# Optimization experiments

Measured on AMD Instinct MI355X. Metric: run time of the kernel, lower is better.

Reference implementation:

```python
import jax, jax.numpy as jnp
import numpy as np

B, N, F, FE, H, C = 2, 2048, 128, 8, 4, 64
LEAKY_ALPHA = 0.2
NEG_INF = -1e9


def setup_inputs() -> dict:
    key = jax.random.key(0)
    ks = jax.random.split(key, 8)
    return {
        "X": jax.random.normal(ks[0], (B, N, F), jnp.float32),
        "A": jax.random.uniform(ks[1], (B, N, N), jnp.float32),
        "E": jax.random.normal(ks[2], (B, N, N, FE), jnp.float32),
        "W_edge": jax.random.normal(ks[3], (FE, 1), jnp.float32) * 0.1,
        "b_edge": jnp.zeros((1,), jnp.float32),
        "W_gat": jax.random.normal(ks[4], (H, F, C), jnp.float32) * 0.05,
        "a_src": jax.random.normal(ks[5], (H, C), jnp.float32) * 0.1,
        "a_dst": jax.random.normal(ks[6], (H, C), jnp.float32) * 0.1,
        "b_gat": jnp.zeros((H * C,), jnp.float32),
        "ln_gamma": jnp.ones((H * C,), jnp.float32),
        "ln_beta": jnp.zeros((H * C,), jnp.float32),
    }


def reference(X, A, E, W_edge, b_edge, W_gat, a_src, a_dst, b_gat, ln_gamma, ln_beta):
    # --- edge gate: sigmoid(Dense_1(E)) -> [B,N,N], multiply into adjacency ---
    edge_w = jax.nn.sigmoid(jnp.einsum("bije,eo->bijo", E, W_edge) + b_edge)
    A = A * edge_w[..., 0]  # [B,N,N]

    # --- multi-head dense GAT (spektral GATConv, concat_heads, elu) ---
    h = jnp.einsum("bnf,hfc->bnhc", X, W_gat)  # [B,N,H,C]
    s_src = jnp.einsum("bnhc,hc->bnh", h, a_src)  # [B,N,H]
    s_dst = jnp.einsum("bnhc,hc->bnh", h, a_dst)
    # e_ij = LeakyReLU(src_i + dst_j): [B,N(i),N(j),H]
    logits = jax.nn.leaky_relu(s_src[:, :, None, :] + s_dst[:, None, :, :],
                               negative_slope=LEAKY_ALPHA)
    mask = jnp.where(A == 0.0, NEG_INF, 0.0)[..., None]  # [B,N,N,1]
    attn = jax.nn.softmax(logits + mask, axis=2)  # softmax over neighbors j
    out = jnp.einsum("bijh,bjhc->bihc", attn, h)  # [B,N,H,C]
    out = out.reshape(B, N, H * C) + b_gat
    out = jax.nn.elu(out)

    # --- LayerNorm over the feature axis (inference: dropout is identity) ---
    mu = jnp.mean(out, axis=-1, keepdims=True)
    var = jnp.var(out, axis=-1, keepdims=True)
    out = (out - mu) * jax.lax.rsqrt(var + 1e-3) * ln_gamma + ln_beta
    return out
```

## Files before the change

### kernel.cpp

```cpp
#include <hip/hip_runtime.h>
#include <hip/hip_bf16.h>


#define BB 2
#define NN 2048
#define FF 128
#define HH 4
#define CC 64
#define HC 256
#define TN 8
#define JB (NN / 8)
#define LOG2E 1.4426950408889634f

typedef __attribute__((ext_vector_type(8))) short short8;
typedef __attribute__((ext_vector_type(4))) float f32x4;

__device__ __forceinline__ float wave_sum(float v) {
#pragma unroll
    for (int m = 32; m >= 1; m >>= 1) v += __shfl_xor(v, m, 64);
    return v;
}

__device__ __forceinline__ unsigned short bf16rne(float x) {
    unsigned u = __float_as_uint(x);
    return (unsigned short)((u + 0x7fffu + ((u >> 16) & 1u)) >> 16);
}

__global__ __launch_bounds__(256) void k1_proj(
    const float* __restrict__ X, const float* __restrict__ Adj,
    const float* __restrict__ Wg,
    const float* __restrict__ a_src, const float* __restrict__ a_dst,
    unsigned short* __restrict__ hT, float* __restrict__ ssT,
    float* __restrict__ sdT, unsigned char* __restrict__ zT)
{
    const int blk = blockIdx.x;
    const int b  = blk / (NN / TN);
    const int n0 = (blk % (NN / TN)) * TN;
    const int tid = threadIdx.x;
    const int h = tid >> 6, c = tid & 63;

    float hv[TN];
#pragma unroll
    for (int r = 0; r < TN; ++r) hv[r] = 0.f;

    const float* xp = X + (size_t)(b * NN + n0) * FF;

#pragma unroll 4
    for (int f4 = 0; f4 < FF / 4; ++f4) {
        const int f = f4 * 4;
        const float w0 = Wg[(h * FF + f + 0) * CC + c];
        const float w1 = Wg[(h * FF + f + 1) * CC + c];
        const float w2 = Wg[(h * FF + f + 2) * CC + c];
        const float w3 = Wg[(h * FF + f + 3) * CC + c];
#pragma unroll
        for (int r = 0; r < TN; ++r) {
            float4 x4 = *(const float4*)(xp + r * FF + f);
            hv[r] = fmaf(x4.x, w0, hv[r]);
            hv[r] = fmaf(x4.y, w1, hv[r]);
            hv[r] = fmaf(x4.z, w2, hv[r]);
            hv[r] = fmaf(x4.w, w3, hv[r]);
        }
    }

    union { short8 v; unsigned short u[8]; } pk;
#pragma unroll
    for (int r = 0; r < TN; ++r) pk.u[r] = bf16rne(hv[r]);
    *(short8*)&hT[((((size_t)b * HH + h) * JB + (n0 >> 3)) * CC + c) * 8] = pk.v;

    const float as = a_src[tid];
    const float ad = a_dst[tid];
#pragma unroll
    for (int r = 0; r < TN; ++r) {
        const int n = n0 + r;
        float s1 = wave_sum(hv[r] * as);
        float s2 = wave_sum(hv[r] * ad);
        if (c == 0) {
            ssT[(b * HH + h) * NN + n] = s1 * LOG2E;
            sdT[(b * HH + h) * NN + n] = s2 * LOG2E;
        }
    }

    {
        const int r = tid >> 5;
        const int s = tid & 31;
        const size_t row = (size_t)(b * NN + n0 + r);
        const float* ap = Adj + row * NN + s * 64;
        unsigned char* zp = zT + (row << 8);
#pragma unroll
        for (int k = 0; k < 8; ++k) {
            float4 a0 = *(const float4*)(ap + k * 8);
            float4 a1 = *(const float4*)(ap + k * 8 + 4);
            unsigned m = 0u;
            m |= (a0.x == 0.f) ? 1u   : 0u;
            m |= (a0.y == 0.f) ? 2u   : 0u;
            m |= (a0.z == 0.f) ? 4u   : 0u;
            m |= (a0.w == 0.f) ? 8u   : 0u;
            m |= (a1.x == 0.f) ? 16u  : 0u;
            m |= (a1.y == 0.f) ? 32u  : 0u;
            m |= (a1.z == 0.f) ? 64u  : 0u;
            m |= (a1.w == 0.f) ? 128u : 0u;
            const int jb = s * 8 + k;
            const int jq = jb >> 6, rem = jb & 63;
            const int it = rem >> 2, lq = rem & 3;
            zp[jq * 64 + lq * 16 + it] = (unsigned char)m;
        }
    }
}

struct Stage {
    float4 sda, sdb;
    short8 bfr[4];
};

__device__ __forceinline__ void load_stage(
    Stage& s, const float* sdp, const unsigned short* hb, int it)
{
    const int js = it * 32;
    s.sda = *(const float4*)(sdp + js);
    s.sdb = *(const float4*)(sdp + js + 4);
    const unsigned short* hp = hb + it * 2048;
#pragma unroll
    for (int ni = 0; ni < 4; ++ni)
        s.bfr[ni] = *(const short8*)(hp + ni * 128);
}

__device__ __forceinline__ void consume_stage(
    const Stage& s, float ss, bool wz,
    unsigned long long mlo, unsigned long long mhi, int it,
    f32x4* acc, f32x4& accS, short8 onesv)
{
    const float sd[8] = {s.sda.x, s.sda.y, s.sda.z, s.sda.w,
                         s.sdb.x, s.sdb.y, s.sdb.z, s.sdb.w};
    float p[8];
    __builtin_amdgcn_s_setprio(1);
#pragma unroll
    for (int t = 0; t < 8; ++t) {
        float x = ss + sd[t];
        x = fmaxf(x, 0.2f * x);
        p[t] = __builtin_amdgcn_exp2f(x);
    }
    if (wz) {
        const unsigned mb =
            (unsigned)(((it & 8) ? mhi : mlo) >> ((it & 7) * 8)) & 0xffu;
        if (__any(mb != 0u)) {
#pragma unroll
            for (int t = 0; t < 8; ++t)
                if ((mb >> t) & 1u) p[t] = 0.f;
        }
    }
    union { short8 v; __hip_bfloat162 h2[4]; } pk;
#pragma unroll
    for (int t = 0; t < 4; ++t)
        pk.h2[t] = __float22bfloat162_rn(make_float2(p[2 * t], p[2 * t + 1]));
    accS = __builtin_amdgcn_mfma_f32_16x16x32_bf16(pk.v, onesv, accS, 0, 0, 0);
#pragma unroll
    for (int ni = 0; ni < 4; ++ni)
        acc[ni] = __builtin_amdgcn_mfma_f32_16x16x32_bf16(pk.v, s.bfr[ni], acc[ni], 0, 0, 0);
    __builtin_amdgcn_s_setprio(0);
}

__global__ __launch_bounds__(1024, 4) void k2_attn(
    const unsigned short* __restrict__ hT, const float* __restrict__ ssT,
    const float* __restrict__ sdT, const unsigned char* __restrict__ zT,
    float* __restrict__ Pacc, float* __restrict__ Pden)
{
    const int blk = blockIdx.x;
    const int b     = blk >> 7;
    const int itile = (blk >> 2) & 31;
    const int jqB   = blk & 3;
    const int i0    = itile * 64;
    const int tid  = threadIdx.x;
    const int wave = tid >> 6;
    const int h    = wave & 3;
    const int isub = wave >> 2;
    const int l  = tid & 63;
    const int lr = l & 15;
    const int lq = l >> 4;
    const int irow0 = i0 + isub * 16;

    const float ss = ssT[(b * HH + h) * NN + irow0 + lr];

    const uint4 mw = *(const uint4*)(zT + ((size_t)(b * NN + irow0 + lr) << 8)
                                       + jqB * 64 + lq * 16);
    const unsigned long long mlo = ((unsigned long long)mw.y << 32) | mw.x;
    const unsigned long long mhi = ((unsigned long long)mw.w << 32) | mw.z;
    const bool wz = __any((mlo | mhi) != 0ull);

    short8 onesv;
#pragma unroll
    for (int i = 0; i < 8; ++i) onesv[i] = (short)0x3F80;

    f32x4 acc[4];
#pragma unroll
    for (int ni = 0; ni < 4; ++ni) acc[ni] = (f32x4){0.f, 0.f, 0.f, 0.f};
    f32x4 accS = (f32x4){0.f, 0.f, 0.f, 0.f};

    const float* sdp = sdT + (b * HH + h) * NN + jqB * 512 + lq * 8;
    const unsigned short* hb =
        hT + ((((size_t)b * HH + h) * JB + jqB * 64 + lq) * CC + lr) * 8;

    Stage s0, s1;
    load_stage(s0, sdp, hb, 0);
    load_stage(s1, sdp, hb, 1);
#pragma unroll 1
    for (int it = 0; it < 16; it += 2) {
        consume_stage(s0, ss, wz, mlo, mhi, it, acc, accS, onesv);
        if (it + 2 < 16) load_stage(s0, sdp, hb, it + 2);
        consume_stage(s1, ss, wz, mlo, mhi, it + 1, acc, accS, onesv);
        if (it + 3 < 16) load_stage(s1, sdp, hb, it + 3);
    }

    float* pa = Pacc + (((size_t)(b * 4 + jqB) * NN + irow0) * HC) + h * 64 + lr;
#pragma unroll
    for (int ni = 0; ni < 4; ++ni)
#pragma unroll
        for (int r = 0; r < 4; ++r)
            pa[(size_t)(lq * 4 + r) * HC + ni * 16] = acc[ni][r];
    if (lr == 0) {
        float* pd = Pden + ((size_t)(b * 4 + jqB) * NN + irow0) * HH + h;
#pragma unroll
        for (int r = 0; r < 4; ++r) pd[(lq * 4 + r) * HH] = accS[r];
    }
}

__global__ __launch_bounds__(256) void k3_norm(
    const float* __restrict__ Pacc, const float* __restrict__ Pden,
    const float* __restrict__ b_gat, const float* __restrict__ gamma,
    const float* __restrict__ beta, float* __restrict__ out)
{
    const int blk = blockIdx.x;
    const int b  = blk >> 7;
    const int i0 = (blk & 127) << 4;
    const int tid = threadIdx.x;
    const int row = tid >> 4;
    const int q   = tid & 15;
    const int i   = i0 + row;
    const int h   = q >> 2;

    float4 s[4];
#pragma unroll
    for (int k = 0; k < 4; ++k) s[k] = make_float4(0.f, 0.f, 0.f, 0.f);
    float d = 0.f;

#pragma unroll
    for (int jq = 0; jq < 4; ++jq) {
        const float* pa = Pacc + ((size_t)(b * 4 + jq) * NN + i) * HC + q * 16;
#pragma unroll
        for (int k = 0; k < 4; ++k) {
            float4 v = *(const float4*)(pa + k * 4);
            s[k].x += v.x; s[k].y += v.y; s[k].z += v.z; s[k].w += v.w;
        }
        d += Pden[((size_t)(b * 4 + jq) * NN + i) * HH + h];
    }

    const float invd = 1.f / d;
    float vv[16];
    float S1 = 0.f, S2 = 0.f;
#pragma unroll
    for (int k = 0; k < 4; ++k) {
        float4 bg = *(const float4*)(b_gat + q * 16 + k * 4);
        float e[4] = {s[k].x, s[k].y, s[k].z, s[k].w};
        float g[4] = {bg.x, bg.y, bg.z, bg.w};
#pragma unroll
        for (int t = 0; t < 4; ++t) {
            float v = e[t] * invd + g[t];
            v = (v > 0.f) ? v : (__expf(v) - 1.f);
            vv[k * 4 + t] = v;
            S1 += v;
            S2 += v * v;
        }
    }
#pragma unroll
    for (int m = 1; m <= 8; m <<= 1) {
        S1 += __shfl_xor(S1, m, 64);
        S2 += __shfl_xor(S2, m, 64);
    }
    const float mu  = S1 * (1.f / HC);
    const float var = S2 * (1.f / HC) - mu * mu;
    const float inv = rsqrtf(var + 1e-3f);

    float* op = out + (size_t)(b * NN + i) * HC + q * 16;
#pragma unroll
    for (int k = 0; k < 4; ++k) {
        float4 gm = *(const float4*)(gamma + q * 16 + k * 4);
        float4 bm = *(const float4*)(beta  + q * 16 + k * 4);
        float4 o;
        o.x = (vv[k * 4 + 0] - mu) * inv * gm.x + bm.x;
        o.y = (vv[k * 4 + 1] - mu) * inv * gm.y + bm.y;
        o.z = (vv[k * 4 + 2] - mu) * inv * gm.z + bm.z;
        o.w = (vv[k * 4 + 3] - mu) * inv * gm.w + bm.w;
        *(float4*)(op + k * 4) = o;
    }
}

extern "C" void kernel_launch(void* const* d_in, const int* in_sizes, int n_in,
                              void* d_out, int out_size, void* d_ws, size_t ws_size,
                              hipStream_t stream)
{
    const float* X     = (const float*)d_in[0];
    const float* Adj   = (const float*)d_in[1];
    const float* Wg    = (const float*)d_in[5];
    const float* a_src = (const float*)d_in[6];
    const float* a_dst = (const float*)d_in[7];
    const float* b_gat = (const float*)d_in[8];
    const float* gam   = (const float*)d_in[9];
    const float* bet   = (const float*)d_in[10];
    float* out = (float*)d_out;

    const size_t hT_elems = (size_t)BB * HH * CC * NN;
    const size_t ss_elems = (size_t)BB * HH * NN;
    const size_t zT_bytes = (size_t)BB * NN * 256;

    unsigned short* hT = (unsigned short*)d_ws;
    float* ssT = (float*)(hT + hT_elems);
    float* sdT = ssT + ss_elems;
    unsigned char* zT = (unsigned char*)(sdT + ss_elems);
    float* Pacc = (float*)(zT + zT_bytes);
    float* Pden = Pacc + (size_t)BB * 4 * NN * HC;

    k1_proj<<<BB * NN / TN, 256, 0, stream>>>(X, Adj, Wg, a_src, a_dst, hT, ssT, sdT, zT);
    k2_attn<<<BB * (NN / 16), 1024, 0, stream>>>(hT, ssT, sdT, zT, Pacc, Pden);
    k3_norm<<<BB * (NN / 16), 256, 0, stream>>>(Pacc, Pden, b_gat, gam, bet, out);
}
```

Before: 375.8 us.

## Process two row tiles per wave and reduce j-quarters in shared memory

```diff
diff --git a/kernel.cpp b/kernel.cpp
--- a/kernel.cpp
+++ b/kernel.cpp
@@ -124,102 +124,165 @@
         s.bfr[ni] = *(const short8*)(hp + ni * 128);
 }
 
-__device__ __forceinline__ void consume_stage(
-    const Stage& s, float ss, bool wz,
-    unsigned long long mlo, unsigned long long mhi, int it,
-    f32x4* acc, f32x4& accS, short8 onesv)
+__device__ __forceinline__ void consume2(
+    const Stage& s, float ss0, float ss1, bool wz,
+    unsigned mb0, unsigned mb1,
+    f32x4* acc0, f32x4* acc1, f32x4& accS0, f32x4& accS1, short8 onesv)
 {
     const float sd[8] = {s.sda.x, s.sda.y, s.sda.z, s.sda.w,
                          s.sdb.x, s.sdb.y, s.sdb.z, s.sdb.w};
-    float p[8];
+    float p0[8], p1[8];
     __builtin_amdgcn_s_setprio(1);
 #pragma unroll
     for (int t = 0; t < 8; ++t) {
-        float x = ss + sd[t];
-        x = fmaxf(x, 0.2f * x);
-        p[t] = __builtin_amdgcn_exp2f(x);
+        float x0 = ss0 + sd[t];
+        x0 = fmaxf(x0, 0.2f * x0);
+        p0[t] = __builtin_amdgcn_exp2f(x0);
+        float x1 = ss1 + sd[t];
+        x1 = fmaxf(x1, 0.2f * x1);
+        p1[t] = __builtin_amdgcn_exp2f(x1);
     }
     if (wz) {
-        const unsigned mb =
-            (unsigned)(((it & 8) ? mhi : mlo) >> ((it & 7) * 8)) & 0xffu;
-        if (__any(mb != 0u)) {
-#pragma unroll
-            for (int t = 0; t < 8; ++t)
-                if ((mb >> t) & 1u) p[t] = 0.f;
-        }
-    }
-    union { short8 v; __hip_bfloat162 h2[4]; } pk;
-#pragma unroll
-    for (int t = 0; t < 4; ++t)
-        pk.h2[t] = __float22bfloat162_rn(make_float2(p[2 * t], p[2 * t + 1]));
-    accS = __builtin_amdgcn_mfma_f32_16x16x32_bf16(pk.v, onesv, accS, 0, 0, 0);
-#pragma unroll
-    for (int ni = 0; ni < 4; ++ni)
-        acc[ni] = __builtin_amdgcn_mfma_f32_16x16x32_bf16(pk.v, s.bfr[ni], acc[ni], 0, 0, 0);
+        if (__any((mb0 | mb1) != 0u)) {
+#pragma unroll
+            for (int t = 0; t < 8; ++t) {
+                if ((mb0 >> t) & 1u) p0[t] = 0.f;
+                if ((mb1 >> t) & 1u) p1[t] = 0.f;
+            }
+        }
+    }
+    union { short8 v; __hip_bfloat162 h2[4]; } pk0, pk1;
+#pragma unroll
+    for (int t = 0; t < 4; ++t) {
+        pk0.h2[t] = __float22bfloat162_rn(make_float2(p0[2 * t], p0[2 * t + 1]));
+        pk1.h2[t] = __float22bfloat162_rn(make_float2(p1[2 * t], p1[2 * t + 1]));
+    }
+    accS0 = __builtin_amdgcn_mfma_f32_16x16x32_bf16(pk0.v, onesv, accS0, 0, 0, 0);
+    accS1 = __builtin_amdgcn_mfma_f32_16x16x32_bf16(pk1.v, onesv, accS1, 0, 0, 0);
+#pragma unroll
+    for (int ni = 0; ni < 4; ++ni) {
+        acc0[ni] = __builtin_amdgcn_mfma_f32_16x16x32_bf16(pk0.v, s.bfr[ni], acc0[ni], 0, 0, 0);
+        acc1[ni] = __builtin_amdgcn_mfma_f32_16x16x32_bf16(pk1.v, s.bfr[ni], acc1[ni], 0, 0, 0);
+    }
     __builtin_amdgcn_s_setprio(0);
 }
 
-__global__ __launch_bounds__(1024, 4) void k2_attn(
+__global__ __launch_bounds__(1024, 2) void k2_attn(
     const unsigned short* __restrict__ hT, const float* __restrict__ ssT,
     const float* __restrict__ sdT, const unsigned char* __restrict__ zT,
     float* __restrict__ Pacc, float* __restrict__ Pden)
 {
+    __shared__ float accs[HH][32][64];
+    __shared__ float lsb[HH][32];
+
     const int blk = blockIdx.x;
     const int b     = blk >> 7;
-    const int itile = (blk >> 2) & 31;
-    const int jqB   = blk & 3;
-    const int i0    = itile * 64;
+    const int itile = (blk >> 1) & 63;
+    const int jh    = blk & 1;
+    const int i0    = itile * 32;
     const int tid  = threadIdx.x;
     const int wave = tid >> 6;
-    const int h    = wave & 3;
-    const int isub = wave >> 2;
+    const int h  = wave & 3;
+    const int jq = wave >> 2;
     const int l  = tid & 63;
     const int lr = l & 15;
     const int lq = l >> 4;
-    const int irow0 = i0 + isub * 16;
-
-    const float ss = ssT[(b * HH + h) * NN + irow0 + lr];
-
-    const uint4 mw = *(const uint4*)(zT + ((size_t)(b * NN + irow0 + lr) << 8)
-                                       + jqB * 64 + lq * 16);
-    const unsigned long long mlo = ((unsigned long long)mw.y << 32) | mw.x;
-    const unsigned long long mhi = ((unsigned long long)mw.w << 32) | mw.z;
-    const bool wz = __any((mlo | mhi) != 0ull);
+
+    const int row0 = i0 + lr, row1 = i0 + 16 + lr;
+    const float ss0 = ssT[(b * HH + h) * NN + row0];
+    const float ss1 = ssT[(b * HH + h) * NN + row1];
+
+    const size_t zoff = (size_t)((jh * 2 + (jq >> 1)) * 64 + lq * 16 + (jq & 1) * 8);
+    const uint2 mz0 = *(const uint2*)(zT + (((size_t)(b * NN + row0)) << 8) + zoff);
+    const uint2 mz1 = *(const uint2*)(zT + (((size_t)(b * NN + row1)) << 8) + zoff);
+    const unsigned long long m0 = ((unsigned long long)mz0.y << 32) | mz0.x;
+    const unsigned long long m1 = ((unsigned long long)mz1.y << 32) | mz1.x;
+    const bool wz = __any((m0 | m1) != 0ull);
 
     short8 onesv;
 #pragma unroll
     for (int i = 0; i < 8; ++i) onesv[i] = (short)0x3F80;
 
-    f32x4 acc[4];
-#pragma unroll
-    for (int ni = 0; ni < 4; ++ni) acc[ni] = (f32x4){0.f, 0.f, 0.f, 0.f};
-    f32x4 accS = (f32x4){0.f, 0.f, 0.f, 0.f};
-
-    const float* sdp = sdT + (b * HH + h) * NN + jqB * 512 + lq * 8;
+    f32x4 acc0[4], acc1[4];
+#pragma unroll
+    for (int ni = 0; ni < 4; ++ni) {
+        acc0[ni] = (f32x4){0.f, 0.f, 0.f, 0.f};
+        acc1[ni] = (f32x4){0.f, 0.f, 0.f, 0.f};
+    }
+    f32x4 accS0 = (f32x4){0.f, 0.f, 0.f, 0.f};
+    f32x4 accS1 = (f32x4){0.f, 0.f, 0.f, 0.f};
+
+    const float* sdp = sdT + (b * HH + h) * NN + jh * 1024 + jq * 256 + lq * 8;
     const unsigned short* hb =
-        hT + ((((size_t)b * HH + h) * JB + jqB * 64 + lq) * CC + lr) * 8;
+        hT + ((((size_t)b * HH + h) * JB + jh * 128 + jq * 32 + lq) * CC + lr) * 8;
 
     Stage s0, s1;
     load_stage(s0, sdp, hb, 0);
     load_stage(s1, sdp, hb, 1);
 #pragma unroll 1
-    for (int it = 0; it < 16; it += 2) {
-        consume_stage(s0, ss, wz, mlo, mhi, it, acc, accS, onesv);
-        if (it + 2 < 16) load_stage(s0, sdp, hb, it + 2);
-        consume_stage(s1, ss, wz, mlo, mhi, it + 1, acc, accS, onesv);
-        if (it + 3 < 16) load_stage(s1, sdp, hb, it + 3);
-    }
-
-    float* pa = Pacc + (((size_t)(b * 4 + jqB) * NN + irow0) * HC) + h * 64 + lr;
-#pragma unroll
-    for (int ni = 0; ni < 4; ++ni)
-#pragma unroll
-        for (int r = 0; r < 4; ++r)
-            pa[(size_t)(lq * 4 + r) * HC + ni * 16] = acc[ni][r];
-    if (lr == 0) {
-        float* pd = Pden + ((size_t)(b * 4 + jqB) * NN + irow0) * HH + h;
-#pragma unroll
-        for (int r = 0; r < 4; ++r) pd[(lq * 4 + r) * HH] = accS[r];
+    for (int it = 0; it < 8; it += 2) {
+        const unsigned mb00 = (unsigned)(m0 >> (it * 8)) & 0xffu;
+        const unsigned mb10 = (unsigned)(m1 >> (it * 8)) & 0xffu;
+        const unsigned mb01 = (unsigned)(m0 >> (it * 8 + 8)) & 0xffu;
+        const unsigned mb11 = (unsigned)(m1 >> (it * 8 + 8)) & 0xffu;
+        consume2(s0, ss0, ss1, wz, mb00, mb10, acc0, acc1, accS0, accS1, onesv);
+        if (it + 2 < 8) load_stage(s0, sdp, hb, it + 2);
+        consume2(s1, ss0, ss1, wz, mb01, mb11, acc0, acc1, accS0, accS1, onesv);
+        if (it + 3 < 8) load_stage(s1, sdp, hb, it + 3);
+    }
+
+#pragma unroll 1
+    for (int rnd = 1; rnd <= 3; ++rnd) {
+        if (jq == rnd) {
+#pragma unroll
+            for (int ni = 0; ni < 4; ++ni)
+#pragma unroll
+                for (int r = 0; r < 4; ++r) {
+                    accs[h][lq * 4 + r][ni * 16 + lr]      = acc0[ni][r];
+                    accs[h][16 + lq * 4 + r][ni * 16 + lr] = acc1[ni][r];
+                }
+            if (lr == 0)
+#pragma unroll
+                for (int r = 0; r < 4; ++r) {
+                    lsb[h][lq * 4 + r]      = accS0[r];
+                    lsb[h][16 + lq * 4 + r] = accS1[r];
+                }
+        }
+        __syncthreads();
+        if (jq == 0) {
+#pragma unroll
+            for (int ni = 0; ni < 4; ++ni)
+#pragma unroll
+                for (int r = 0; r < 4; ++r) {
+                    acc0[ni][r] += accs[h][lq * 4 + r][ni * 16 + lr];
+                    acc1[ni][r] += accs[h][16 + lq * 4 + r][ni * 16 + lr];
+                }
+#pragma unroll
+            for (int r = 0; r < 4; ++r) {
+                accS0[r] += lsb[h][lq * 4 + r];
+                accS1[r] += lsb[h][16 + lq * 4 + r];
+            }
+        }
+        __syncthreads();
+    }
+
+    if (jq == 0) {
+        float* pa = Pacc + ((size_t)(jh * BB + b) * NN + i0) * HC + h * 64 + lr;
+#pragma unroll
+        for (int ni = 0; ni < 4; ++ni)
+#pragma unroll
+            for (int r = 0; r < 4; ++r) {
+                pa[(size_t)(lq * 4 + r) * HC + ni * 16]      = acc0[ni][r];
+                pa[(size_t)(16 + lq * 4 + r) * HC + ni * 16] = acc1[ni][r];
+            }
+        if (lr == 0) {
+            float* pd = Pden + ((size_t)(jh * BB + b) * NN + i0) * HH + h;
+#pragma unroll
+            for (int r = 0; r < 4; ++r) {
+                pd[(lq * 4 + r) * HH]      = accS0[r];
+                pd[(16 + lq * 4 + r) * HH] = accS1[r];
+            }
+        }
     }
 }
 
@@ -243,14 +306,14 @@
     float d = 0.f;
 
 #pragma unroll
-    for (int jq = 0; jq < 4; ++jq) {
-        const float* pa = Pacc + ((size_t)(b * 4 + jq) * NN + i) * HC + q * 16;
+    for (int jh = 0; jh < 2; ++jh) {
+        const float* pa = Pacc + ((size_t)(jh * BB + b) * NN + i) * HC + q * 16;
 #pragma unroll
         for (int k = 0; k < 4; ++k) {
             float4 v = *(const float4*)(pa + k * 4);
             s[k].x += v.x; s[k].y += v.y; s[k].z += v.z; s[k].w += v.w;
         }
-        d += Pden[((size_t)(b * 4 + jq) * NN + i) * HH + h];
+        d += Pden[((size_t)(jh * BB + b) * NN + i) * HH + h];
     }
 
     const float invd = 1.f / d;
@@ -316,7 +379,7 @@
     float* sdT = ssT + ss_elems;
     unsigned char* zT = (unsigned char*)(sdT + ss_elems);
     float* Pacc = (float*)(zT + zT_bytes);
-    float* Pden = Pacc + (size_t)BB * 4 * NN * HC;
+    float* Pden = Pacc + (size_t)2 * BB * NN * HC;
 
     k1_proj<<<BB * NN / TN, 256, 0, stream>>>(X, Adj, Wg, a_src, a_dst, hT, ssT, sdT, zT);
     k2_attn<<<BB * (NN / 16), 1024, 0, stream>>>(hT, ssT, sdT, zT, Pacc, Pden);
```

Result: no change. 372.4 us (-0.9%).
